# Kernel optimization log

Hardware: AMD Instinct MI355X
Metric: run time of the kernel (lower is better)

The kernel has to match this reference:

```python
import math
import jax, jax.numpy as jnp
import numpy as np

N_NODES = 10000
N_EDGES = 160000
F_IN = 256
HID = 500
N_OUT = 100


def setup_inputs() -> dict:
    key = jax.random.key(0)
    ks = jax.random.split(key, 20)
    inp = {}
    inp['x'] = jax.random.normal(ks[0], (N_NODES, F_IN), jnp.float32)
    inp['edge_src'] = jax.random.randint(ks[1], (N_EDGES,), 0, N_NODES, jnp.int32)
    inp['edge_dst'] = jax.random.randint(ks[2], (N_EDGES,), 0, N_NODES, jnp.int32)
    inp['edge_weight'] = jax.random.uniform(ks[3], (N_EDGES,), jnp.float32)
    s1 = 1.0 / math.sqrt(F_IN)
    s2 = 1.0 / math.sqrt(HID)
    inp['W1_rel'] = jax.random.uniform(ks[4], (HID, F_IN), jnp.float32, -s1, s1)
    inp['b1'] = jax.random.uniform(ks[5], (HID,), jnp.float32, -s1, s1)
    inp['W1_root'] = jax.random.uniform(ks[6], (HID, F_IN), jnp.float32, -s1, s1)
    inp['p1_w'] = jax.random.uniform(ks[7], (HID,), jnp.float32, -s2, s2)
    inp['W2_rel'] = jax.random.uniform(ks[8], (HID, HID), jnp.float32, -s2, s2)
    inp['b2'] = jax.random.uniform(ks[9], (HID,), jnp.float32, -s2, s2)
    inp['W2_root'] = jax.random.uniform(ks[10], (HID, HID), jnp.float32, -s2, s2)
    inp['p2_w'] = jax.random.uniform(ks[11], (HID,), jnp.float32, -s2, s2)
    s3 = 1.0 / math.sqrt(1000)
    inp['lin1_W'] = jax.random.uniform(ks[12], (2000, 1000), jnp.float32, -s3, s3)
    inp['lin1_b'] = jax.random.uniform(ks[13], (2000,), jnp.float32, -s3, s3)
    s4 = 1.0 / math.sqrt(2000)
    inp['lin2_W'] = jax.random.uniform(ks[14], (4000, 2000), jnp.float32, -s4, s4)
    inp['lin2_b'] = jax.random.uniform(ks[15], (4000,), jnp.float32, -s4, s4)
    s5 = 1.0 / math.sqrt(4000)
    inp['lin3_W'] = jax.random.uniform(ks[16], (N_OUT, 4000), jnp.float32, -s5, s5)
    inp['lin3_b'] = jax.random.uniform(ks[17], (N_OUT,), jnp.float32, -s5, s5)
    return inp


def graph_conv(x, src, dst, w, W_rel, b_rel, W_root):
    # PyG GraphConv: out_i = W_rel @ sum_{j->i} w_ji * x_j + b + W_root @ x_i
    msg = x[src] * w[:, None]                              # [E, F]
    agg = jax.ops.segment_sum(msg, dst, num_segments=x.shape[0])
    return agg @ W_rel.T + b_rel + x @ W_root.T


def topk_pool(x, src, dst, w, p_w, ratio=0.5):
    # PyG TopKPooling: score = tanh(x @ p / ||p||); keep top-k; scale x by score.
    N = x.shape[0]
    k = int(math.ceil(ratio * N))
    score = jnp.tanh((x @ p_w) / jnp.linalg.norm(p_w))
    vals, perm = jax.lax.top_k(score, k)
    x_new = x[perm] * vals[:, None]
    # keep fixed-size edge list; dropped edges get weight 0 and point to node 0
    new_idx = jnp.zeros((N,), jnp.int32).at[perm].set(jnp.arange(k, dtype=jnp.int32))
    mask = jnp.zeros((N,), bool).at[perm].set(True)
    keep = mask[src] & mask[dst]
    src_new = jnp.where(keep, new_idx[src], 0)
    dst_new = jnp.where(keep, new_idx[dst], 0)
    w_new = jnp.where(keep, w, 0.0)
    return x_new, src_new, dst_new, w_new


def readout(x):
    # global max pool + global mean pool over the single graph -> [1, 2F]
    return jnp.concatenate([jnp.max(x, 0, keepdims=True), jnp.mean(x, 0, keepdims=True)], axis=1)


def reference(x, edge_src, edge_dst, edge_weight,
              W1_rel, b1, W1_root, p1_w,
              W2_rel, b2, W2_root, p2_w,
              lin1_W, lin1_b, lin2_W, lin2_b, lin3_W, lin3_b):
    h = jax.nn.relu(graph_conv(x, edge_src, edge_dst, edge_weight, W1_rel, b1, W1_root))
    h, s1, d1, w1 = topk_pool(h, edge_src, edge_dst, edge_weight, p1_w)
    x1 = readout(h)
    h = jax.nn.relu(graph_conv(h, s1, d1, w1, W2_rel, b2, W2_root))
    h, _, _, _ = topk_pool(h, s1, d1, w1, p2_w)
    x2 = readout(h)
    z = x1 + x2                                            # [1, 1000]
    z = jax.nn.relu(z @ lin1_W.T + lin1_b)
    z = jax.nn.relu(z @ lin2_W.T + lin2_b)                 # dropout is identity at eval
    return jax.nn.sigmoid(z @ lin3_W.T + lin3_b)
```

## Files before the change

kernel.cpp:

```cpp
#include <hip/hip_runtime.h>
#include <hip/hip_bf16.h>
#include <math.h>

#define NN1   10000
#define NE    160000
#define FIN   256
#define HID   500
#define K1    5000
#define NN2   5000
#define K2    2500

#define CSR_OFFS   0u
#define CSR_POS    10008u
#define CSR_EDGE   20008u
#define OFF_AGG    340016u
#define OFF_H      2900016u
#define OFF_XP2    (OFF_H + 2500000u)
#define OFF_SCP    7900016u
#define OFF_RK1    10410016u
#define OFF_Z      10432016u
#define OFF_T1     10433016u
#define OFF_T2     10435016u
#define OFF_INV    10439016u
#define OFF_CNT    10439024u
#define OFF_PM1    10639024u
#define OFF_PS1    10671024u
#define OFF_XB     10703024u
#define OFF_W1RB   11983024u
#define OFF_W1TB   12047024u
#define OFF_W2RB   12111024u
#define OFF_W2TB   12236024u
#define OFF_XP1B   12361024u
#define OFF_PM2    13611024u
#define OFF_PS2    13627024u
#define WS_FLOATS  13643024u

#define RCHUNK 500
#define ROSLAB1 64
#define ROSLAB2 32
#define RORPB   79

__device__ inline unsigned f2ord(float f) {
    unsigned u = __float_as_uint(f);
    return (u & 0x80000000u) ? ~u : (u | 0x80000000u);
}
__device__ inline unsigned long long rkey(float s, int j) {
    return ((unsigned long long)f2ord(s) << 32) | (unsigned)(0xFFFFFFFFu - (unsigned)j);
}
__device__ inline unsigned short bf16rn(float f) {
    unsigned u = __float_as_uint(f);
    u += 0x7FFFu + ((u >> 16) & 1u);
    return (unsigned short)(u >> 16);
}
__device__ inline float bf2f(unsigned short u) {
    return __uint_as_float((unsigned)u << 16);
}

typedef __attribute__((ext_vector_type(8))) short short8;
typedef __attribute__((ext_vector_type(4))) float floatx4;


__global__ __launch_bounds__(256) void k_prep(
    const float* __restrict__ x, unsigned short* __restrict__ xb,
    const float* __restrict__ w1r, unsigned short* __restrict__ w1rb,
    const float* __restrict__ w1t, unsigned short* __restrict__ w1tb,
    const float* __restrict__ w2r, unsigned short* __restrict__ w2rb,
    const float* __restrict__ w2t, unsigned short* __restrict__ w2tb,
    const float* __restrict__ p1, const float* __restrict__ p2,
    float* __restrict__ invn,
    const int* __restrict__ edst, int* __restrict__ pos) {
    __shared__ float red[256];
    int y = blockIdx.y;
    if (y < 5) {
        const float* s; unsigned short* d; int n;
        switch (y) {
            case 0: s = x;   d = xb;   n = NN1 * FIN; break;
            case 1: s = w1r; d = w1rb; n = HID * FIN; break;
            case 2: s = w1t; d = w1tb; n = HID * FIN; break;
            case 3: s = w2r; d = w2rb; n = HID * HID; break;
            default: s = w2t; d = w2tb; n = HID * HID; break;
        }
        int i = (blockIdx.x * 256 + threadIdx.x) * 4;
        if (i >= n) return;
        if (i + 3 < n) {
            float4 v = *(const float4*)(s + i);
            ushort4 o;
            o.x = bf16rn(v.x); o.y = bf16rn(v.y); o.z = bf16rn(v.z); o.w = bf16rn(v.w);
            *(ushort4*)(d + i) = o;
        } else {
            for (int q = 0; q < 4 && i + q < n; ++q) d[i + q] = bf16rn(s[i + q]);
        }
    } else if (y == 5) {
        if (blockIdx.x >= 2) return;
        const float* p = blockIdx.x ? p2 : p1;
        float s = 0.f;
        for (int i = threadIdx.x; i < HID; i += 256) { float v = p[i]; s += v * v; }
        red[threadIdx.x] = s; __syncthreads();
        for (int w = 128; w > 0; w >>= 1) {
            if (threadIdx.x < w) red[threadIdx.x] += red[threadIdx.x + w];
            __syncthreads();
        }
        if (threadIdx.x == 0) invn[blockIdx.x] = 1.0f / sqrtf(red[0]);
    } else {
        int e = blockIdx.x * 256 + threadIdx.x;
        if (e < NE) atomicAdd(&pos[edst[e]], 1);
    }
}

__global__ __launch_bounds__(1024) void k_scan(int* __restrict__ pos, int* __restrict__ offs) {
    __shared__ int tot[1024];
    int t = threadIdx.x;
    int base = t * 10;
    int loc[10]; int s = 0;
    #pragma unroll
    for (int q = 0; q < 10; ++q) {
        int v = (base + q < NN1) ? pos[base + q] : 0;
        loc[q] = s; s += v;
    }
    tot[t] = s; __syncthreads();
    for (int d = 1; d < 1024; d <<= 1) {
        int v = (t >= d) ? tot[t - d] : 0;
        __syncthreads();
        tot[t] += v;
        __syncthreads();
    }
    int excl = (t == 0) ? 0 : tot[t - 1];
    #pragma unroll
    for (int q = 0; q < 10; ++q)
        if (base + q < NN1) { int o = excl + loc[q]; offs[base + q] = o; pos[base + q] = o; }
    if (t == 1023) offs[NN1] = tot[1023];
}

__global__ void k_fill(const int* __restrict__ src, const int* __restrict__ dst,
                       const float* __restrict__ w, int* __restrict__ pos,
                       int2* __restrict__ ce) {
    int e = blockIdx.x * 256 + threadIdx.x;
    if (e >= NE) return;
    int slot = atomicAdd(&pos[dst[e]], 1);
    ce[slot] = make_int2(src[e], __float_as_int(w[e]));
}

__global__ __launch_bounds__(256) void k_gather1(
    const unsigned short* __restrict__ xb, const int* __restrict__ offs,
    const int2* __restrict__ ce, unsigned short* __restrict__ aggb) {
    int wave = (blockIdx.x * 256 + threadIdx.x) >> 6;
    int lane = threadIdx.x & 63;
    if (wave >= NN1) return;
    int b = offs[wave], e = offs[wave + 1];
    float4 a0 = make_float4(0.f, 0.f, 0.f, 0.f);
    float4 a1 = make_float4(0.f, 0.f, 0.f, 0.f);
    int p = b;
    for (; p + 1 < e; p += 2) {
        int2 e0 = ce[p], e1 = ce[p + 1];
        float w0 = __int_as_float(e0.y), w1 = __int_as_float(e1.y);
        ushort4 u0 = *(const ushort4*)(xb + (size_t)e0.x * FIN + lane * 4);
        ushort4 u1 = *(const ushort4*)(xb + (size_t)e1.x * FIN + lane * 4);
        a0.x += bf2f(u0.x) * w0; a0.y += bf2f(u0.y) * w0;
        a0.z += bf2f(u0.z) * w0; a0.w += bf2f(u0.w) * w0;
        a1.x += bf2f(u1.x) * w1; a1.y += bf2f(u1.y) * w1;
        a1.z += bf2f(u1.z) * w1; a1.w += bf2f(u1.w) * w1;
    }
    if (p < e) {
        int2 e0 = ce[p];
        float w0 = __int_as_float(e0.y);
        ushort4 u0 = *(const ushort4*)(xb + (size_t)e0.x * FIN + lane * 4);
        a0.x += bf2f(u0.x) * w0; a0.y += bf2f(u0.y) * w0;
        a0.z += bf2f(u0.z) * w0; a0.w += bf2f(u0.w) * w0;
    }
    ushort4 o;
    o.x = bf16rn(a0.x + a1.x); o.y = bf16rn(a0.y + a1.y);
    o.z = bf16rn(a0.z + a1.z); o.w = bf16rn(a0.w + a1.w);
    *(ushort4*)(aggb + (size_t)wave * FIN + lane * 4) = o;
}

__global__ __launch_bounds__(256) void k_gather2(
    const unsigned short* __restrict__ Xb, const int* __restrict__ offs,
    const int2* __restrict__ ce, const int* __restrict__ rank,
    unsigned short* __restrict__ aggb) {
    int wave = (blockIdx.x * 256 + threadIdx.x) >> 6;
    int lane = threadIdx.x & 63;
    if (wave >= NN1) return;
    int rd = rank[wave];
    if (rd < 0) return;
    int b = offs[wave], e = offs[wave + 1];
    int c1 = 256 + lane * 4;
    float a0 = 0.f, a1 = 0.f, a2 = 0.f, a3 = 0.f;
    float b0 = 0.f, b1v = 0.f, b2 = 0.f, b3 = 0.f;
    int2 nxt = (b < e) ? ce[b] : make_int2(0, 0);
    for (int p = b; p < e; ++p) {
        int2 cur = nxt;
        if (p + 1 < e) nxt = ce[p + 1];
        int rs = rank[cur.x];
        if (rs < 0) continue;
        float we = __int_as_float(cur.y);
        const unsigned short* row = Xb + (size_t)rs * HID;
        ushort4 u = *(const ushort4*)(row + lane * 4);
        a0 += bf2f(u.x) * we; a1 += bf2f(u.y) * we;
        a2 += bf2f(u.z) * we; a3 += bf2f(u.w) * we;
        if (c1 < HID) {
            ushort4 u2 = *(const ushort4*)(row + c1);
            b0 += bf2f(u2.x) * we; b1v += bf2f(u2.y) * we;
            b2 += bf2f(u2.z) * we; b3 += bf2f(u2.w) * we;
        }
    }
    unsigned short* o = aggb + (size_t)rd * HID;
    ushort4 o1; o1.x = bf16rn(a0); o1.y = bf16rn(a1); o1.z = bf16rn(a2); o1.w = bf16rn(a3);
    *(ushort4*)(o + lane * 4) = o1;
    if (c1 < HID) {
        ushort4 o2; o2.x = bf16rn(b0); o2.y = bf16rn(b1v); o2.z = bf16rn(b2); o2.w = bf16rn(b3);
        *(ushort4*)(o + c1) = o2;
    }
}

__device__ inline short8 ld8g(const unsigned short* p, int gk, int K) {
    if (gk + 7 < K) return *(const short8*)p;
    unsigned short tmp[8] = {0,0,0,0,0,0,0,0};
    for (int q = 0; q < 8; ++q) if (gk + q < K) tmp[q] = p[q];
    return *(short8*)tmp;
}

#define GBK 64
__global__ __launch_bounds__(256) void k_gemm_bf16(
    const unsigned short* __restrict__ A1, const unsigned short* __restrict__ B1,
    const unsigned short* __restrict__ A2, const unsigned short* __restrict__ B2,
    const float* __restrict__ bias, const float* __restrict__ pv,
    unsigned short* __restrict__ C, float* __restrict__ scpart,
    int M, int N, int Ka, int Kb, int nbyRow) {
    int b = blockIdx.x;
    int xcd = b & 7, seq = b >> 3;
    int colT = seq & 7;
    int rowT = xcd + 8 * (seq >> 3);
    if (rowT >= nbyRow) return;
    int row0 = rowT * 64, col0 = colT * 64;

    __shared__ unsigned short As[2][64 * 64];
    __shared__ unsigned short Bs[2][64 * 64];
    int tid = threadIdx.x;
    int lane = tid & 63, wid = tid >> 6;
    int waveM = wid & 1, waveN = wid >> 1;
    int quad = lane >> 4, mrow = lane & 15;
    int m7 = mrow & 7;
    floatx4 acc[2][2] = {};

    int sr = tid >> 2;
    int ca = (tid & 3) * 2;
    int s7 = sr & 7;
    int c0 = (ca ^ s7) * 8;
    int c1 = ((ca + 1) ^ s7) * 8;
    int sbase = sr * 64;

    int nka = (Ka + GBK - 1) / GBK;
    int nkb = (Kb + GBK - 1) / GBK;
    int niter = nka + nkb;

    short8 z8 = {0,0,0,0,0,0,0,0};
    short8 paA = z8, paB = z8, pbA = z8, pbB = z8;

    auto fetch = [&](int t) {
        int ph = (t >= nka);
        const unsigned short* A = ph ? A2 : A1;
        const unsigned short* B = ph ? B2 : B1;
        int K = ph ? Kb : Ka;
        int gk = (ph ? t - nka : t) * GBK + ca * 8;
        int gr = row0 + sr, gn = col0 + sr;
        paA = z8; paB = z8; pbA = z8; pbB = z8;
        if (gr < M) {
            const unsigned short* p = A + (size_t)gr * K + gk;
            paA = ld8g(p, gk, K); paB = ld8g(p + 8, gk + 8, K);
        }
        if (gn < N) {
            const unsigned short* p = B + (size_t)gn * K + gk;
            pbA = ld8g(p, gk, K); pbB = ld8g(p + 8, gk + 8, K);
        }
    };
    auto commit = [&](int buf) {
        *(short8*)&As[buf][sbase + c0] = paA;
        *(short8*)&As[buf][sbase + c1] = paB;
        *(short8*)&Bs[buf][sbase + c0] = pbA;
        *(short8*)&Bs[buf][sbase + c1] = pbB;
    };

    fetch(0);
    commit(0);
    if (niter > 1) fetch(1);
    __syncthreads();

    for (int it = 0; it < niter; ++it) {
        int cur = it & 1;
        if (it + 1 < niter) commit(cur ^ 1);
        if (it + 2 < niter) fetch(it + 2);
        #pragma unroll
        for (int half = 0; half < 2; ++half) {
            int qc = half * 4 + quad;
            int qoff = (qc ^ m7) * 8;
            short8 bfr[2];
            #pragma unroll
            for (int nt = 0; nt < 2; ++nt)
                bfr[nt] = *(short8*)&Bs[cur][(waveN * 32 + nt * 16 + mrow) * 64 + qoff];
            #pragma unroll
            for (int mt = 0; mt < 2; ++mt) {
                short8 afr = *(short8*)&As[cur][(waveM * 32 + mt * 16 + mrow) * 64 + qoff];
                #pragma unroll
                for (int nt = 0; nt < 2; ++nt)
                    acc[mt][nt] = __builtin_amdgcn_mfma_f32_16x16x32_bf16(
                        afr, bfr[nt], acc[mt][nt], 0, 0, 0);
            }
        }
        __syncthreads();
    }
    float ps[2][4] = {};
    #pragma unroll
    for (int nt = 0; nt < 2; ++nt) {
        int col = col0 + waveN * 32 + nt * 16 + mrow;
        if (col >= N) continue;
        float bv = bias[col];
        float pc = pv[col];
        #pragma unroll
        for (int mt = 0; mt < 2; ++mt) {
            int rbase = row0 + waveM * 32 + mt * 16 + quad * 4;
            #pragma unroll
            for (int r = 0; r < 4; ++r) {
                float v = fmaxf(acc[mt][nt][r] + bv, 0.f);
                int row = rbase + r;
                if (row < M) C[(size_t)row * N + col] = bf16rn(v);
                ps[mt][r] += v * pc;
            }
        }
    }
    int part = colT * 2 + waveN;
    #pragma unroll
    for (int mt = 0; mt < 2; ++mt)
        #pragma unroll
        for (int r = 0; r < 4; ++r) {
            float v = ps[mt][r];
            v += __shfl_xor(v, 1, 64); v += __shfl_xor(v, 2, 64);
            v += __shfl_xor(v, 4, 64); v += __shfl_xor(v, 8, 64);
            if (mrow == 0) {
                int row = row0 + waveM * 32 + mt * 16 + quad * 4 + r;
                if (row < M) scpart[(size_t)part * M + row] = v;
            }
        }
}

__global__ __launch_bounds__(256) void k_rank_partial(
    const float* __restrict__ scpart, int* __restrict__ cntp, int Nn) {
    __shared__ unsigned long long kj[RCHUNK];
    int j0 = blockIdx.y * RCHUNK;
    int jn = min(Nn - j0, RCHUNK);
    for (int t = threadIdx.x; t < jn; t += 256) {
        float s = 0.f;
        #pragma unroll
        for (int q = 0; q < 16; ++q) s += scpart[(size_t)q * Nn + j0 + t];
        kj[t] = rkey(s, j0 + t);
    }
    __syncthreads();
    int i = blockIdx.x * 256 + threadIdx.x;
    if (i >= Nn) return;
    float si = 0.f;
    #pragma unroll
    for (int q = 0; q < 16; ++q) si += scpart[(size_t)q * Nn + i];
    unsigned long long ki = rkey(si, i);
    int c = 0;
    #pragma unroll 4
    for (int q = 0; q < jn; ++q)
        c += (kj[q] > ki) ? 1 : 0;
    cntp[(size_t)blockIdx.y * Nn + i] = c;
}

__global__ __launch_bounds__(128) void k_gather_pool(
    const unsigned short* __restrict__ Hb, const float* __restrict__ scpart,
    const float* __restrict__ invn,
    const int* __restrict__ cntp, int Nn, int nchunk, int kk,
    int* __restrict__ rank_out, unsigned short* __restrict__ Xb) {
    __shared__ int csum[128];
    __shared__ float ssum[128];
    __shared__ int rsh;
    __shared__ float scsh;
    int i = blockIdx.x;
    int c = 0;
    for (int q = threadIdx.x; q < nchunk; q += 128) c += cntp[(size_t)q * Nn + i];
    float s = (threadIdx.x < 16) ? scpart[(size_t)threadIdx.x * Nn + i] : 0.f;
    csum[threadIdx.x] = c; ssum[threadIdx.x] = s;
    __syncthreads();
    if (threadIdx.x == 0) {
        int t = 0;
        int lim = (nchunk < 128) ? nchunk : 128;
        for (int q = 0; q < lim; ++q) t += csum[q];
        float st = 0.f;
        for (int q = 0; q < 16; ++q) st += ssum[q];
        int r = (t < kk) ? t : -1;
        if (rank_out) rank_out[i] = r;
        rsh = r;
        scsh = tanhf(st * invn[0]);
    }
    __syncthreads();
    int r = rsh;
    if (r < 0) return;
    float sc = scsh;
    int cc = threadIdx.x;
    if (cc < HID / 4) {
        ushort4 u = *(const ushort4*)(Hb + (size_t)i * HID + cc * 4);
        ushort4 o;
        o.x = bf16rn(bf2f(u.x) * sc); o.y = bf16rn(bf2f(u.y) * sc);
        o.z = bf16rn(bf2f(u.z) * sc); o.w = bf16rn(bf2f(u.w) * sc);
        *(ushort4*)(Xb + (size_t)r * HID + cc * 4) = o;
    }
}

__global__ __launch_bounds__(256) void k_readout_slab(
    const unsigned short* __restrict__ X, int rows, int rpb,
    float* __restrict__ pmax, float* __restrict__ psum) {
    __shared__ float4 lmx[4][64];
    __shared__ float4 lsm[4][64];
    int lane = threadIdx.x & 63;
    int rgrp = threadIdx.x >> 6;
    int c4 = blockIdx.x * 64 + lane;
    int r0 = blockIdx.y * rpb;
    int r1 = min(rows, r0 + rpb);
    float4 mx = make_float4(-INFINITY, -INFINITY, -INFINITY, -INFINITY);
    float4 sm = make_float4(0.f, 0.f, 0.f, 0.f);
    if (c4 < HID / 4) {
        for (int r = r0 + rgrp; r < r1; r += 4) {
            ushort4 u = *(const ushort4*)(X + (size_t)r * HID + c4 * 4);
            float vx = bf2f(u.x), vy = bf2f(u.y), vz = bf2f(u.z), vw = bf2f(u.w);
            mx.x = fmaxf(mx.x, vx); mx.y = fmaxf(mx.y, vy);
            mx.z = fmaxf(mx.z, vz); mx.w = fmaxf(mx.w, vw);
            sm.x += vx; sm.y += vy; sm.z += vz; sm.w += vw;
        }
    }
    lmx[rgrp][lane] = mx; lsm[rgrp][lane] = sm;
    __syncthreads();
    if (rgrp == 0 && c4 < HID / 4) {
        #pragma unroll
        for (int g = 1; g < 4; ++g) {
            float4 m2 = lmx[g][lane], s2 = lsm[g][lane];
            mx.x = fmaxf(mx.x, m2.x); mx.y = fmaxf(mx.y, m2.y);
            mx.z = fmaxf(mx.z, m2.z); mx.w = fmaxf(mx.w, m2.w);
            sm.x += s2.x; sm.y += s2.y; sm.z += s2.z; sm.w += s2.w;
        }
        *(float4*)(pmax + (size_t)blockIdx.y * HID + c4 * 4) = mx;
        *(float4*)(psum + (size_t)blockIdx.y * HID + c4 * 4) = sm;
    }
}

__global__ __launch_bounds__(64) void k_combine_all(
    const float* __restrict__ pm1, const float* __restrict__ ps1, int ns1,
    const float* __restrict__ pm2, const float* __restrict__ ps2, int ns2,
    float* __restrict__ z) {
    int j = blockIdx.x * 64 + threadIdx.x;
    if (j >= HID) return;
    float m1 = -INFINITY, s1 = 0.f;
    for (int s = 0; s < ns1; ++s) {
        m1 = fmaxf(m1, pm1[(size_t)s * HID + j]);
        s1 += ps1[(size_t)s * HID + j];
    }
    float m2 = -INFINITY, s2 = 0.f;
    for (int s = 0; s < ns2; ++s) {
        m2 = fmaxf(m2, pm2[(size_t)s * HID + j]);
        s2 += ps2[(size_t)s * HID + j];
    }
    z[j] = m1 + m2;
    z[HID + j] = s1 * (1.0f / (float)K1) + s2 * (1.0f / (float)K2);
}

__global__ __launch_bounds__(256) void k_mv(
    const float* __restrict__ v, const float* __restrict__ W,
    const float* __restrict__ bias, float* __restrict__ y,
    int rowsN, int K, int act) {
    int wave = (blockIdx.x * 256 + threadIdx.x) >> 6;
    int lane = threadIdx.x & 63;
    if (wave >= rowsN) return;
    const float* wr = W + (size_t)wave * K;
    float s = 0.f;
    for (int c = lane * 4; c < K; c += 256) {
        float4 a = *(const float4*)(wr + c);
        float4 xv = *(const float4*)(v + c);
        s += a.x * xv.x + a.y * xv.y + a.z * xv.z + a.w * xv.w;
    }
    for (int off = 32; off > 0; off >>= 1) s += __shfl_down(s, off, 64);
    if (lane == 0) {
        float r = s + bias[wave];
        y[wave] = (act == 0) ? fmaxf(r, 0.f) : 1.f / (1.f + expf(-r));
    }
}

extern "C" void kernel_launch(void* const* d_in, const int* in_sizes, int n_in,
                              void* d_out, int out_size, void* d_ws, size_t ws_size,
                              hipStream_t stream) {
    const float* x      = (const float*)d_in[0];
    const int*   esrc   = (const int*)d_in[1];
    const int*   edst   = (const int*)d_in[2];
    const float* ew     = (const float*)d_in[3];
    const float* W1_rel = (const float*)d_in[4];
    const float* b1     = (const float*)d_in[5];
    const float* W1_root= (const float*)d_in[6];
    const float* p1     = (const float*)d_in[7];
    const float* W2_rel = (const float*)d_in[8];
    const float* b2     = (const float*)d_in[9];
    const float* W2_root= (const float*)d_in[10];
    const float* p2     = (const float*)d_in[11];
    const float* l1W    = (const float*)d_in[12];
    const float* l1b    = (const float*)d_in[13];
    const float* l2W    = (const float*)d_in[14];
    const float* l2b    = (const float*)d_in[15];
    const float* l3W    = (const float*)d_in[16];
    const float* l3b    = (const float*)d_in[17];
    float* out = (float*)d_out;
    float* ws  = (float*)d_ws;

    if (ws_size < (size_t)WS_FLOATS * sizeof(float)) return;

    int*            offs  = (int*)(ws + CSR_OFFS);
    int*            pos   = (int*)(ws + CSR_POS);
    int2*           ce    = (int2*)(ws + CSR_EDGE);
    unsigned short* aggb  = (unsigned short*)(ws + OFF_AGG);
    unsigned short* hb    = (unsigned short*)(ws + OFF_H);
    unsigned short* xp2b  = (unsigned short*)(ws + OFF_XP2);
    float*          scp   = ws + OFF_SCP;
    int*            rk1   = (int*)(ws + OFF_RK1);
    float*          zbuf  = ws + OFF_Z;
    float*          t1    = ws + OFF_T1;
    float*          t2    = ws + OFF_T2;
    float*          invn  = ws + OFF_INV;
    int*            cntp  = (int*)(ws + OFF_CNT);
    float*          pm1   = ws + OFF_PM1;
    float*          ps1   = ws + OFF_PS1;
    float*          pm2   = ws + OFF_PM2;
    float*          ps2   = ws + OFF_PS2;
    unsigned short* xb    = (unsigned short*)(ws + OFF_XB);
    unsigned short* w1rb  = (unsigned short*)(ws + OFF_W1RB);
    unsigned short* w1tb  = (unsigned short*)(ws + OFF_W1TB);
    unsigned short* w2rb  = (unsigned short*)(ws + OFF_W2RB);
    unsigned short* w2tb  = (unsigned short*)(ws + OFF_W2TB);
    unsigned short* xp1b  = (unsigned short*)(ws + OFF_XP1B);

    hipMemsetAsync(pos, 0, NN1 * sizeof(int), stream);
    k_prep<<<dim3(2500, 7), 256, 0, stream>>>(
        x, xb, W1_rel, w1rb, W1_root, w1tb, W2_rel, w2rb, W2_root, w2tb,
        p1, p2, invn, edst, pos);
    k_scan<<<1, 1024, 0, stream>>>(pos, offs);
    k_fill<<<(NE + 255) / 256, 256, 0, stream>>>(esrc, edst, ew, pos, ce);

    k_gather1<<<(NN1 * 64 + 255) / 256, 256, 0, stream>>>(xb, offs, ce, aggb);
    {
        int nby = (NN1 + 63) / 64;
        int nblk = 64 * ((nby + 7) / 8);
        k_gemm_bf16<<<nblk, 256, 0, stream>>>(
            aggb, w1rb, xb, w1tb, b1, p1, hb, scp, NN1, HID, FIN, FIN, nby);
    }

    k_rank_partial<<<dim3((NN1 + 255) / 256, NN1 / RCHUNK), 256, 0, stream>>>(scp, cntp, NN1);
    k_gather_pool<<<NN1, 128, 0, stream>>>(hb, scp, invn + 0, cntp, NN1, NN1 / RCHUNK, K1,
                                           rk1, xp1b);
    k_readout_slab<<<dim3(2, ROSLAB1), 256, 0, stream>>>(xp1b, K1, RORPB, pm1, ps1);

    k_gather2<<<(NN1 * 64 + 255) / 256, 256, 0, stream>>>(xp1b, offs, ce, rk1, aggb);
    {
        int nby = (NN2 + 63) / 64;
        int nblk = 64 * ((nby + 7) / 8);
        k_gemm_bf16<<<nblk, 256, 0, stream>>>(
            aggb, w2rb, xp1b, w2tb, b2, p2, hb, scp, NN2, HID, HID, HID, nby);
    }

    k_rank_partial<<<dim3((NN2 + 255) / 256, NN2 / RCHUNK), 256, 0, stream>>>(scp, cntp, NN2);
    k_gather_pool<<<NN2, 128, 0, stream>>>(hb, scp, invn + 1, cntp, NN2, NN2 / RCHUNK, K2,
                                           (int*)nullptr, xp2b);
    k_readout_slab<<<dim3(2, ROSLAB2), 256, 0, stream>>>(xp2b, K2, RORPB, pm2, ps2);
    k_combine_all<<<(HID + 63) / 64, 64, 0, stream>>>(pm1, ps1, ROSLAB1, pm2, ps2, ROSLAB2, zbuf);

    k_mv<<<(2000 * 64) / 256, 256, 0, stream>>>(zbuf, l1W, l1b, t1, 2000, 1000, 0);
    k_mv<<<(4000 * 64) / 256, 256, 0, stream>>>(t1, l2W, l2b, t2, 4000, 2000, 0);
    k_mv<<<(100 * 64) / 256, 256, 0, stream>>>(t2, l3W, l3b, out, 100, 4000, 1);
}
```

Baseline: 329.0 us.

## Fuse pipeline stages into fewer kernels with last-block scans and grid barriers

Folds the degree-count scan into k_prep using a last-block-done counter, removing the separate scan launch. Moves top-k ranking into the GEMM epilogue via a completion counter, and merges gather2 with the layer-1 readout. Collapses pool2, readout2, combine and the three matvecs into one persistent kernel synchronised by software grid barriers. This cuts kernel launches and round trips through memory. The cost is serialised last-block work and grid-barrier overhead, and the barriers depend on all 512 blocks being resident at once to avoid deadlock.

```diff
diff --git a/kernel.cpp b/kernel.cpp
--- a/kernel.cpp
+++ b/kernel.cpp
@@ -1,5 +1,4 @@
 #include <hip/hip_runtime.h>
-#include <hip/hip_bf16.h>
 #include <math.h>
 
 #define NN1   10000
@@ -9,36 +8,40 @@
 #define K1    5000
 #define NN2   5000
 #define K2    2500
+#define NSLAB 64
+#define RORPB  79
+#define RORPB2 40
 
 #define CSR_OFFS   0u
 #define CSR_POS    10008u
-#define CSR_EDGE   20008u
-#define OFF_AGG    340016u
-#define OFF_H      2900016u
-#define OFF_XP2    (OFF_H + 2500000u)
-#define OFF_SCP    7900016u
-#define OFF_RK1    10410016u
-#define OFF_Z      10432016u
-#define OFF_T1     10433016u
-#define OFF_T2     10435016u
-#define OFF_INV    10439016u
-#define OFF_CNT    10439024u
-#define OFF_PM1    10639024u
-#define OFF_PS1    10671024u
-#define OFF_XB     10703024u
-#define OFF_W1RB   11983024u
-#define OFF_W1TB   12047024u
-#define OFF_W2RB   12111024u
-#define OFF_W2TB   12236024u
-#define OFF_XP1B   12361024u
-#define OFF_PM2    13611024u
-#define OFF_PS2    13627024u
-#define WS_FLOATS  13643024u
-
-#define RCHUNK 500
-#define ROSLAB1 64
-#define ROSLAB2 32
-#define RORPB   79
+#define OFF_SC1    20008u
+#define OFF_SC2    30008u
+#define OFF_CTR    35008u
+#define ZERO_BASE  10008u
+#define ZERO_LEN   25032u
+#define CSR_EDGE   35040u
+#define OFF_SCALE1 355040u
+#define OFF_SCALE2 365040u
+#define OFF_RK1    370040u
+#define OFF_RK2    380040u
+#define OFF_PM1    385056u
+#define OFF_PS1    417056u
+#define OFF_PM2    449056u
+#define OFF_PS2    481056u
+#define OFF_Z      513056u
+#define OFF_T1     514056u
+#define OFF_T2     516056u
+#define OFF_INV    520056u
+#define OFF_AGG    520064u
+#define OFF_H      1800064u
+#define OFF_XP1B   4300064u
+#define OFF_XP2B   5550064u
+#define OFF_XB     6175064u
+#define OFF_W1RB   7455064u
+#define OFF_W1TB   7519064u
+#define OFF_W2RB   7583064u
+#define OFF_W2TB   7708064u
+#define WS_FLOATS  7833088u
 
 __device__ inline unsigned f2ord(float f) {
     unsigned u = __float_as_uint(f);
@@ -58,6 +61,13 @@
 
 typedef __attribute__((ext_vector_type(8))) short short8;
 typedef __attribute__((ext_vector_type(4))) float floatx4;
+
+__device__ inline short8 ld8g(const unsigned short* p, int gk, int K) {
+    if (gk + 7 < K) return *(const short8*)p;
+    unsigned short tmp[8] = {0,0,0,0,0,0,0,0};
+    for (int q = 0; q < 8; ++q) if (gk + q < K) tmp[q] = p[q];
+    return *(short8*)tmp;
+}
 
 
 __global__ __launch_bounds__(256) void k_prep(
@@ -68,72 +78,76 @@
     const float* __restrict__ w2t, unsigned short* __restrict__ w2tb,
     const float* __restrict__ p1, const float* __restrict__ p2,
     float* __restrict__ invn,
-    const int* __restrict__ edst, int* __restrict__ pos) {
+    const int* __restrict__ edst, int* __restrict__ pos,
+    int* __restrict__ offs, int* __restrict__ ctr) {
     __shared__ float red[256];
+    __shared__ int ts[264];
+    int tid = threadIdx.x;
     int y = blockIdx.y;
     if (y < 5) {
-        const float* s; unsigned short* d; int n;
+        const float* s; unsigned short* d; int n4;
         switch (y) {
-            case 0: s = x;   d = xb;   n = NN1 * FIN; break;
-            case 1: s = w1r; d = w1rb; n = HID * FIN; break;
-            case 2: s = w1t; d = w1tb; n = HID * FIN; break;
-            case 3: s = w2r; d = w2rb; n = HID * HID; break;
-            default: s = w2t; d = w2tb; n = HID * HID; break;
-        }
-        int i = (blockIdx.x * 256 + threadIdx.x) * 4;
-        if (i >= n) return;
-        if (i + 3 < n) {
-            float4 v = *(const float4*)(s + i);
+            case 0: s = x;   d = xb;   n4 = NN1 * FIN / 4; break;
+            case 1: s = w1r; d = w1rb; n4 = HID * FIN / 4; break;
+            case 2: s = w1t; d = w1tb; n4 = HID * FIN / 4; break;
+            case 3: s = w2r; d = w2rb; n4 = HID * HID / 4; break;
+            default: s = w2t; d = w2tb; n4 = HID * HID / 4; break;
+        }
+        int stride = gridDim.x * 256;
+        for (int i = blockIdx.x * 256 + tid; i < n4; i += stride) {
+            float4 v = *(const float4*)(s + (size_t)i * 4);
             ushort4 o;
             o.x = bf16rn(v.x); o.y = bf16rn(v.y); o.z = bf16rn(v.z); o.w = bf16rn(v.w);
-            *(ushort4*)(d + i) = o;
-        } else {
-            for (int q = 0; q < 4 && i + q < n; ++q) d[i + q] = bf16rn(s[i + q]);
-        }
-    } else if (y == 5) {
-        if (blockIdx.x >= 2) return;
-        const float* p = blockIdx.x ? p2 : p1;
-        float s = 0.f;
-        for (int i = threadIdx.x; i < HID; i += 256) { float v = p[i]; s += v * v; }
-        red[threadIdx.x] = s; __syncthreads();
-        for (int w = 128; w > 0; w >>= 1) {
-            if (threadIdx.x < w) red[threadIdx.x] += red[threadIdx.x + w];
-            __syncthreads();
-        }
-        if (threadIdx.x == 0) invn[blockIdx.x] = 1.0f / sqrtf(red[0]);
-    } else {
-        int e = blockIdx.x * 256 + threadIdx.x;
-        if (e < NE) atomicAdd(&pos[edst[e]], 1);
-    }
-}
-
-__global__ __launch_bounds__(1024) void k_scan(int* __restrict__ pos, int* __restrict__ offs) {
-    __shared__ int tot[1024];
-    int t = threadIdx.x;
-    int base = t * 10;
-    int loc[10]; int s = 0;
-    #pragma unroll
-    for (int q = 0; q < 10; ++q) {
-        int v = (base + q < NN1) ? pos[base + q] : 0;
-        loc[q] = s; s += v;
-    }
-    tot[t] = s; __syncthreads();
-    for (int d = 1; d < 1024; d <<= 1) {
-        int v = (t >= d) ? tot[t - d] : 0;
-        __syncthreads();
-        tot[t] += v;
-        __syncthreads();
-    }
-    int excl = (t == 0) ? 0 : tot[t - 1];
-    #pragma unroll
-    for (int q = 0; q < 10; ++q)
-        if (base + q < NN1) { int o = excl + loc[q]; offs[base + q] = o; pos[base + q] = o; }
-    if (t == 1023) offs[NN1] = tot[1023];
-}
-
-__global__ void k_fill(const int* __restrict__ src, const int* __restrict__ dst,
-                       const float* __restrict__ w, int* __restrict__ pos,
-                       int2* __restrict__ ce) {
+            *(ushort4*)(d + (size_t)i * 4) = o;
+        }
+        return;
+    }
+    if (y == 5) {
+        if (blockIdx.x < 2) {
+            const float* p = blockIdx.x ? p2 : p1;
+            float sv = 0.f;
+            for (int i = tid; i < HID; i += 256) { float v = p[i]; sv += v * v; }
+            red[tid] = sv; __syncthreads();
+            for (int w = 128; w > 0; w >>= 1) {
+                if (tid < w) red[tid] += red[tid + w];
+                __syncthreads();
+            }
+            if (tid == 0) invn[blockIdx.x] = 1.0f / sqrtf(red[0]);
+        }
+        return;
+    }
+    {
+        int stride = gridDim.x * 256;
+        for (int e = blockIdx.x * 256 + tid; e < NE; e += stride)
+            atomicAdd(&pos[edst[e]], 1);
+    }
+    if (tid == 0) {
+        __threadfence();
+        ts[256] = (atomicAdd(ctr, 1) == (int)gridDim.x - 1) ? 1 : 0;
+    }
+    __syncthreads();
+    if (!ts[256]) return;
+    __threadfence();
+    int chunk = (NN1 + 255) / 256;
+    int i0 = tid * chunk, i1 = min(NN1, i0 + chunk);
+    int acc = 0;
+    for (int i = i0; i < i1; ++i) acc += pos[i];
+    ts[tid] = acc; __syncthreads();
+    for (int d = 1; d < 256; d <<= 1) {
+        int v = (tid >= d) ? ts[tid - d] : 0;
+        __syncthreads(); ts[tid] += v; __syncthreads();
+    }
+    int run = tid ? ts[tid - 1] : 0;
+    for (int i = i0; i < i1; ++i) {
+        int v = pos[i]; offs[i] = run; pos[i] = run; run += v;
+    }
+    if (tid == 255) offs[NN1] = ts[255];
+}
+
+__global__ __launch_bounds__(256) void k_fill(
+    const int* __restrict__ src, const int* __restrict__ dst,
+    const float* __restrict__ w, int* __restrict__ pos,
+    int2* __restrict__ ce) {
     int e = blockIdx.x * 256 + threadIdx.x;
     if (e >= NE) return;
     int slot = atomicAdd(&pos[dst[e]], 1);
@@ -173,249 +187,247 @@
     *(ushort4*)(aggb + (size_t)wave * FIN + lane * 4) = o;
 }
 
-__global__ __launch_bounds__(256) void k_gather2(
-    const unsigned short* __restrict__ Xb, const int* __restrict__ offs,
-    const int2* __restrict__ ce, const int* __restrict__ rank,
-    unsigned short* __restrict__ aggb) {
-    int wave = (blockIdx.x * 256 + threadIdx.x) >> 6;
-    int lane = threadIdx.x & 63;
-    if (wave >= NN1) return;
-    int rd = rank[wave];
-    if (rd < 0) return;
-    int b = offs[wave], e = offs[wave + 1];
-    int c1 = 256 + lane * 4;
-    float a0 = 0.f, a1 = 0.f, a2 = 0.f, a3 = 0.f;
-    float b0 = 0.f, b1v = 0.f, b2 = 0.f, b3 = 0.f;
-    int2 nxt = (b < e) ? ce[b] : make_int2(0, 0);
-    for (int p = b; p < e; ++p) {
-        int2 cur = nxt;
-        if (p + 1 < e) nxt = ce[p + 1];
-        int rs = rank[cur.x];
-        if (rs < 0) continue;
-        float we = __int_as_float(cur.y);
-        const unsigned short* row = Xb + (size_t)rs * HID;
-        ushort4 u = *(const ushort4*)(row + lane * 4);
-        a0 += bf2f(u.x) * we; a1 += bf2f(u.y) * we;
-        a2 += bf2f(u.z) * we; a3 += bf2f(u.w) * we;
-        if (c1 < HID) {
-            ushort4 u2 = *(const ushort4*)(row + c1);
-            b0 += bf2f(u2.x) * we; b1v += bf2f(u2.y) * we;
-            b2 += bf2f(u2.z) * we; b3 += bf2f(u2.w) * we;
-        }
-    }
-    unsigned short* o = aggb + (size_t)rd * HID;
-    ushort4 o1; o1.x = bf16rn(a0); o1.y = bf16rn(a1); o1.z = bf16rn(a2); o1.w = bf16rn(a3);
-    *(ushort4*)(o + lane * 4) = o1;
-    if (c1 < HID) {
-        ushort4 o2; o2.x = bf16rn(b0); o2.y = bf16rn(b1v); o2.z = bf16rn(b2); o2.w = bf16rn(b3);
-        *(ushort4*)(o + c1) = o2;
-    }
-}
-
-__device__ inline short8 ld8g(const unsigned short* p, int gk, int K) {
-    if (gk + 7 < K) return *(const short8*)p;
-    unsigned short tmp[8] = {0,0,0,0,0,0,0,0};
-    for (int q = 0; q < 8; ++q) if (gk + q < K) tmp[q] = p[q];
-    return *(short8*)tmp;
-}
-
 #define GBK 64
 __global__ __launch_bounds__(256) void k_gemm_bf16(
     const unsigned short* __restrict__ A1, const unsigned short* __restrict__ B1,
     const unsigned short* __restrict__ A2, const unsigned short* __restrict__ B2,
     const float* __restrict__ bias, const float* __restrict__ pv,
-    unsigned short* __restrict__ C, float* __restrict__ scpart,
+    unsigned short* __restrict__ C, float* __restrict__ score,
+    int* __restrict__ rank_out, float* __restrict__ scale_out,
+    const float* __restrict__ invp, int kk, int* __restrict__ donectr,
     int M, int N, int Ka, int Kb, int nbyRow) {
+    __shared__ unsigned short As[2][64 * 64];
+    __shared__ unsigned short Bs[2][64 * 64];
+    int tid = threadIdx.x;
     int b = blockIdx.x;
     int xcd = b & 7, seq = b >> 3;
     int colT = seq & 7;
     int rowT = xcd + 8 * (seq >> 3);
-    if (rowT >= nbyRow) return;
-    int row0 = rowT * 64, col0 = colT * 64;
-
-    __shared__ unsigned short As[2][64 * 64];
-    __shared__ unsigned short Bs[2][64 * 64];
-    int tid = threadIdx.x;
-    int lane = tid & 63, wid = tid >> 6;
-    int waveM = wid & 1, waveN = wid >> 1;
-    int quad = lane >> 4, mrow = lane & 15;
-    int m7 = mrow & 7;
-    floatx4 acc[2][2] = {};
-
-    int sr = tid >> 2;
-    int ca = (tid & 3) * 2;
-    int s7 = sr & 7;
-    int c0 = (ca ^ s7) * 8;
-    int c1 = ((ca + 1) ^ s7) * 8;
-    int sbase = sr * 64;
-
-    int nka = (Ka + GBK - 1) / GBK;
-    int nkb = (Kb + GBK - 1) / GBK;
-    int niter = nka + nkb;
-
-    short8 z8 = {0,0,0,0,0,0,0,0};
-    short8 paA = z8, paB = z8, pbA = z8, pbB = z8;
-
-    auto fetch = [&](int t) {
-        int ph = (t >= nka);
-        const unsigned short* A = ph ? A2 : A1;
-        const unsigned short* B = ph ? B2 : B1;
-        int K = ph ? Kb : Ka;
-        int gk = (ph ? t - nka : t) * GBK + ca * 8;
-        int gr = row0 + sr, gn = col0 + sr;
-        paA = z8; paB = z8; pbA = z8; pbB = z8;
-        if (gr < M) {
-            const unsigned short* p = A + (size_t)gr * K + gk;
-            paA = ld8g(p, gk, K); paB = ld8g(p + 8, gk + 8, K);
-        }
-        if (gn < N) {
-            const unsigned short* p = B + (size_t)gn * K + gk;
-            pbA = ld8g(p, gk, K); pbB = ld8g(p + 8, gk + 8, K);
-        }
-    };
-    auto commit = [&](int buf) {
-        *(short8*)&As[buf][sbase + c0] = paA;
-        *(short8*)&As[buf][sbase + c1] = paB;
-        *(short8*)&Bs[buf][sbase + c0] = pbA;
-        *(short8*)&Bs[buf][sbase + c1] = pbB;
-    };
-
-    fetch(0);
-    commit(0);
-    if (niter > 1) fetch(1);
-    __syncthreads();
-
-    for (int it = 0; it < niter; ++it) {
-        int cur = it & 1;
-        if (it + 1 < niter) commit(cur ^ 1);
-        if (it + 2 < niter) fetch(it + 2);
+    bool active = (rowT < nbyRow);
+    if (active) {
+        int row0 = rowT * 64, col0 = colT * 64;
+        int lane = tid & 63, wid = tid >> 6;
+        int waveM = wid & 1, waveN = wid >> 1;
+        int quad = lane >> 4, mrow = lane & 15;
+        int m7 = mrow & 7;
+        floatx4 acc[2][2] = {};
+
+        int sr = tid >> 2;
+        int ca = (tid & 3) * 2;
+        int s7 = sr & 7;
+        int c0 = (ca ^ s7) * 8;
+        int c1 = ((ca + 1) ^ s7) * 8;
+        int sbase = sr * 64;
+
+        int nka = (Ka + GBK - 1) / GBK;
+        int nkb = (Kb + GBK - 1) / GBK;
+        int niter = nka + nkb;
+
+        short8 z8 = {0,0,0,0,0,0,0,0};
+        short8 paA = z8, paB = z8, pbA = z8, pbB = z8;
+
+        auto fetch = [&](int t) {
+            int ph = (t >= nka);
+            const unsigned short* A = ph ? A2 : A1;
+            const unsigned short* B = ph ? B2 : B1;
+            int K = ph ? Kb : Ka;
+            int gk = (ph ? t - nka : t) * GBK + ca * 8;
+            int gr = row0 + sr, gn = col0 + sr;
+            paA = z8; paB = z8; pbA = z8; pbB = z8;
+            if (gr < M) {
+                const unsigned short* p = A + (size_t)gr * K + gk;
+                paA = ld8g(p, gk, K); paB = ld8g(p + 8, gk + 8, K);
+            }
+            if (gn < N) {
+                const unsigned short* p = B + (size_t)gn * K + gk;
+                pbA = ld8g(p, gk, K); pbB = ld8g(p + 8, gk + 8, K);
+            }
+        };
+        auto commit = [&](int buf) {
+            *(short8*)&As[buf][sbase + c0] = paA;
+            *(short8*)&As[buf][sbase + c1] = paB;
+            *(short8*)&Bs[buf][sbase + c0] = pbA;
+            *(short8*)&Bs[buf][sbase + c1] = pbB;
+        };
+
+        fetch(0);
+        commit(0);
+        if (niter > 1) fetch(1);
+        __syncthreads();
+
+        for (int it = 0; it < niter; ++it) {
+            int cur = it & 1;
+            if (it + 1 < niter) commit(cur ^ 1);
+            if (it + 2 < niter) fetch(it + 2);
+            #pragma unroll
+            for (int half = 0; half < 2; ++half) {
+                int qc = half * 4 + quad;
+                int qoff = (qc ^ m7) * 8;
+                short8 bfr[2];
+                #pragma unroll
+                for (int nt = 0; nt < 2; ++nt)
+                    bfr[nt] = *(short8*)&Bs[cur][(waveN * 32 + nt * 16 + mrow) * 64 + qoff];
+                #pragma unroll
+                for (int mt = 0; mt < 2; ++mt) {
+                    short8 afr = *(short8*)&As[cur][(waveM * 32 + mt * 16 + mrow) * 64 + qoff];
+                    #pragma unroll
+                    for (int nt = 0; nt < 2; ++nt)
+                        acc[mt][nt] = __builtin_amdgcn_mfma_f32_16x16x32_bf16(
+                            afr, bfr[nt], acc[mt][nt], 0, 0, 0);
+                }
+            }
+            __syncthreads();
+        }
+        float ps[2][4] = {};
         #pragma unroll
-        for (int half = 0; half < 2; ++half) {
-            int qc = half * 4 + quad;
-            int qoff = (qc ^ m7) * 8;
-            short8 bfr[2];
-            #pragma unroll
-            for (int nt = 0; nt < 2; ++nt)
-                bfr[nt] = *(short8*)&Bs[cur][(waveN * 32 + nt * 16 + mrow) * 64 + qoff];
+        for (int nt = 0; nt < 2; ++nt) {
+            int col = col0 + waveN * 32 + nt * 16 + mrow;
+            if (col >= N) continue;
+            float bv = bias[col];
+            float pc = pv[col];
             #pragma unroll
             for (int mt = 0; mt < 2; ++mt) {
-                short8 afr = *(short8*)&As[cur][(waveM * 32 + mt * 16 + mrow) * 64 + qoff];
+                int rbase = row0 + waveM * 32 + mt * 16 + quad * 4;
                 #pragma unroll
-                for (int nt = 0; nt < 2; ++nt)
-                    acc[mt][nt] = __builtin_amdgcn_mfma_f32_16x16x32_bf16(
-                        afr, bfr[nt], acc[mt][nt], 0, 0, 0);
-            }
-        }
-        __syncthreads();
-    }
-    float ps[2][4] = {};
-    #pragma unroll
-    for (int nt = 0; nt < 2; ++nt) {
-        int col = col0 + waveN * 32 + nt * 16 + mrow;
-        if (col >= N) continue;
-        float bv = bias[col];
-        float pc = pv[col];
+                for (int r = 0; r < 4; ++r) {
+                    float v = fmaxf(acc[mt][nt][r] + bv, 0.f);
+                    int row = rbase + r;
+                    if (row < M) C[(size_t)row * N + col] = bf16rn(v);
+                    ps[mt][r] += v * pc;
+                }
+            }
+        }
         #pragma unroll
-        for (int mt = 0; mt < 2; ++mt) {
-            int rbase = row0 + waveM * 32 + mt * 16 + quad * 4;
+        for (int mt = 0; mt < 2; ++mt)
             #pragma unroll
             for (int r = 0; r < 4; ++r) {
-                float v = fmaxf(acc[mt][nt][r] + bv, 0.f);
-                int row = rbase + r;
-                if (row < M) C[(size_t)row * N + col] = bf16rn(v);
-                ps[mt][r] += v * pc;
-            }
-        }
-    }
-    int part = colT * 2 + waveN;
-    #pragma unroll
-    for (int mt = 0; mt < 2; ++mt)
-        #pragma unroll
-        for (int r = 0; r < 4; ++r) {
-            float v = ps[mt][r];
-            v += __shfl_xor(v, 1, 64); v += __shfl_xor(v, 2, 64);
-            v += __shfl_xor(v, 4, 64); v += __shfl_xor(v, 8, 64);
-            if (mrow == 0) {
-                int row = row0 + waveM * 32 + mt * 16 + quad * 4 + r;
-                if (row < M) scpart[(size_t)part * M + row] = v;
-            }
-        }
-}
-
-__global__ __launch_bounds__(256) void k_rank_partial(
-    const float* __restrict__ scpart, int* __restrict__ cntp, int Nn) {
-    __shared__ unsigned long long kj[RCHUNK];
-    int j0 = blockIdx.y * RCHUNK;
-    int jn = min(Nn - j0, RCHUNK);
-    for (int t = threadIdx.x; t < jn; t += 256) {
-        float s = 0.f;
-        #pragma unroll
-        for (int q = 0; q < 16; ++q) s += scpart[(size_t)q * Nn + j0 + t];
-        kj[t] = rkey(s, j0 + t);
-    }
-    __syncthreads();
-    int i = blockIdx.x * 256 + threadIdx.x;
-    if (i >= Nn) return;
-    float si = 0.f;
-    #pragma unroll
-    for (int q = 0; q < 16; ++q) si += scpart[(size_t)q * Nn + i];
-    unsigned long long ki = rkey(si, i);
-    int c = 0;
-    #pragma unroll 4
-    for (int q = 0; q < jn; ++q)
-        c += (kj[q] > ki) ? 1 : 0;
-    cntp[(size_t)blockIdx.y * Nn + i] = c;
-}
-
-__global__ __launch_bounds__(128) void k_gather_pool(
-    const unsigned short* __restrict__ Hb, const float* __restrict__ scpart,
-    const float* __restrict__ invn,
-    const int* __restrict__ cntp, int Nn, int nchunk, int kk,
-    int* __restrict__ rank_out, unsigned short* __restrict__ Xb) {
-    __shared__ int csum[128];
-    __shared__ float ssum[128];
-    __shared__ int rsh;
-    __shared__ float scsh;
+                float v = ps[mt][r];
+                v += __shfl_xor(v, 1, 64); v += __shfl_xor(v, 2, 64);
+                v += __shfl_xor(v, 4, 64); v += __shfl_xor(v, 8, 64);
+                if (mrow == 0) {
+                    int row = row0 + waveM * 32 + mt * 16 + quad * 4 + r;
+                    if (row < M) atomicAdd(&score[row], v);
+                }
+            }
+    }
+
+    int* hist = (int*)(void*)As[0];
+    int* ts   = (int*)(void*)As[1];
+    unsigned long long* keys = (unsigned long long*)(void*)Bs[0];
+    if (tid == 0) {
+        __threadfence();
+        ts[270] = (atomicAdd(donectr, 1) == (int)gridDim.x - 1) ? 1 : 0;
+    }
+    __syncthreads();
+    if (!ts[270]) return;
+    __threadfence();
+
+    unsigned prefMask = 0, prefVal = 0;
+    int need = kk;
+    int cnt = M;
+    const int shifts[3] = {21, 10, 0};
+    const int nbits[3]  = {11, 11, 10};
+    for (int lv = 0; lv < 3 && cnt > 2048; ++lv) {
+        int sh = shifts[lv], nb = 1 << nbits[lv], per = nb >> 8;
+        for (int q = tid; q < nb; q += 256) hist[q] = 0;
+        __syncthreads();
+        for (int i = tid; i < M; i += 256) {
+            unsigned key = f2ord(score[i]);
+            if ((key & prefMask) == prefVal)
+                atomicAdd(&hist[(key >> sh) & (nb - 1)], 1);
+        }
+        __syncthreads();
+        int c = 0;
+        int btop = nb - 1 - tid * per;
+        for (int j = 0; j < per; ++j) c += hist[btop - j];
+        ts[tid] = c; __syncthreads();
+        for (int d = 1; d < 256; d <<= 1) {
+            int v = (tid >= d) ? ts[tid - d] : 0;
+            __syncthreads(); ts[tid] += v; __syncthreads();
+        }
+        int above = tid ? ts[tid - 1] : 0;
+        int cum = above;
+        for (int j = 0; j < per; ++j) {
+            int bb = btop - j; int h = hist[bb];
+            if (cum < need && need <= cum + h) { ts[260] = bb; ts[261] = cum; }
+            cum += h;
+        }
+        __syncthreads();
+        int B = ts[260], abv = ts[261];
+        need -= abv;
+        cnt = hist[B];
+        prefMask |= (unsigned)(nb - 1) << sh;
+        prefVal  |= (unsigned)B << sh;
+        __syncthreads();
+    }
+    if (tid == 0) ts[262] = 0;
+    __syncthreads();
+    for (int i = tid; i < M; i += 256) {
+        float s = score[i];
+        unsigned key = f2ord(s);
+        if ((key & prefMask) == prefVal) {
+            int p = atomicAdd(&ts[262], 1);
+            if (p < 2048) keys[p] = rkey(s, i);
+        }
+    }
+    __syncthreads();
+    int m = ts[262]; if (m > 2048) m = 2048;
+    for (int c = tid; c < m; c += 256) {
+        unsigned long long kc = keys[c];
+        int rk = 0;
+        for (int q = 0; q < m; ++q) rk += (keys[q] > kc) ? 1 : 0;
+        if (rk == need - 1) {
+            ts[263] = (int)(unsigned)(kc & 0xFFFFFFFFull);
+            ts[264] = (int)(unsigned)(kc >> 32);
+        }
+    }
+    __syncthreads();
+    unsigned long long thr =
+        ((unsigned long long)(unsigned)ts[264] << 32) | (unsigned)ts[263];
+    float inv = invp[0];
+    int chunk = (M + 255) / 256;
+    int i0 = tid * chunk, i1 = min(M, i0 + chunk);
+    int ck = 0;
+    for (int i = i0; i < i1; ++i) ck += (rkey(score[i], i) >= thr) ? 1 : 0;
+    ts[tid] = ck; __syncthreads();
+    for (int d = 1; d < 256; d <<= 1) {
+        int v = (tid >= d) ? ts[tid - d] : 0;
+        __syncthreads(); ts[tid] += v; __syncthreads();
+    }
+    int r = tid ? ts[tid - 1] : 0;
+    for (int i = i0; i < i1; ++i) {
+        float s = score[i];
+        bool kept = rkey(s, i) >= thr;
+        rank_out[i] = kept ? r++ : -1;
+        scale_out[i] = tanhf(s * inv);
+    }
+}
+
+__global__ __launch_bounds__(128) void k_pool_gather(
+    const unsigned short* __restrict__ Hb, const int* __restrict__ rank,
+    const float* __restrict__ scale, unsigned short* __restrict__ Xb) {
     int i = blockIdx.x;
-    int c = 0;
-    for (int q = threadIdx.x; q < nchunk; q += 128) c += cntp[(size_t)q * Nn + i];
-    float s = (threadIdx.x < 16) ? scpart[(size_t)threadIdx.x * Nn + i] : 0.f;
-    csum[threadIdx.x] = c; ssum[threadIdx.x] = s;
-    __syncthreads();
-    if (threadIdx.x == 0) {
-        int t = 0;
-        int lim = (nchunk < 128) ? nchunk : 128;
-        for (int q = 0; q < lim; ++q) t += csum[q];
-        float st = 0.f;
-        for (int q = 0; q < 16; ++q) st += ssum[q];
-        int r = (t < kk) ? t : -1;
-        if (rank_out) rank_out[i] = r;
-        rsh = r;
-        scsh = tanhf(st * invn[0]);
-    }
-    __syncthreads();
-    int r = rsh;
+    int r = rank[i];
     if (r < 0) return;
-    float sc = scsh;
     int cc = threadIdx.x;
-    if (cc < HID / 4) {
-        ushort4 u = *(const ushort4*)(Hb + (size_t)i * HID + cc * 4);
-        ushort4 o;
-        o.x = bf16rn(bf2f(u.x) * sc); o.y = bf16rn(bf2f(u.y) * sc);
-        o.z = bf16rn(bf2f(u.z) * sc); o.w = bf16rn(bf2f(u.w) * sc);
-        *(ushort4*)(Xb + (size_t)r * HID + cc * 4) = o;
-    }
-}
-
-__global__ __launch_bounds__(256) void k_readout_slab(
-    const unsigned short* __restrict__ X, int rows, int rpb,
-    float* __restrict__ pmax, float* __restrict__ psum) {
+    if (cc >= HID / 4) return;
+    float sc = scale[i];
+    ushort4 u = *(const ushort4*)(Hb + (size_t)i * HID + cc * 4);
+    ushort4 o;
+    o.x = bf16rn(bf2f(u.x) * sc); o.y = bf16rn(bf2f(u.y) * sc);
+    o.z = bf16rn(bf2f(u.z) * sc); o.w = bf16rn(bf2f(u.w) * sc);
+    *(ushort4*)(Xb + (size_t)r * HID + cc * 4) = o;
+}
+
+__device__ void readout_slab(const unsigned short* __restrict__ X, int rows, int rpb,
+                             int slabY, int colHalf,
+                             float* __restrict__ pmax, float* __restrict__ psum) {
     __shared__ float4 lmx[4][64];
     __shared__ float4 lsm[4][64];
     int lane = threadIdx.x & 63;
     int rgrp = threadIdx.x >> 6;
-    int c4 = blockIdx.x * 64 + lane;
-    int r0 = blockIdx.y * rpb;
+    int c4 = colHalf * 64 + lane;
+    int r0 = slabY * rpb;
     int r1 = min(rows, r0 + rpb);
     float4 mx = make_float4(-INFINITY, -INFINITY, -INFINITY, -INFINITY);
     float4 sm = make_float4(0.f, 0.f, 0.f, 0.f);
@@ -438,50 +450,148 @@
             mx.z = fmaxf(mx.z, m2.z); mx.w = fmaxf(mx.w, m2.w);
             sm.x += s2.x; sm.y += s2.y; sm.z += s2.z; sm.w += s2.w;
         }
-        *(float4*)(pmax + (size_t)blockIdx.y * HID + c4 * 4) = mx;
-        *(float4*)(psum + (size_t)blockIdx.y * HID + c4 * 4) = sm;
-    }
-}
-
-__global__ __launch_bounds__(64) void k_combine_all(
-    const float* __restrict__ pm1, const float* __restrict__ ps1, int ns1,
-    const float* __restrict__ pm2, const float* __restrict__ ps2, int ns2,
-    float* __restrict__ z) {
-    int j = blockIdx.x * 64 + threadIdx.x;
-    if (j >= HID) return;
-    float m1 = -INFINITY, s1 = 0.f;
-    for (int s = 0; s < ns1; ++s) {
-        m1 = fmaxf(m1, pm1[(size_t)s * HID + j]);
-        s1 += ps1[(size_t)s * HID + j];
-    }
-    float m2 = -INFINITY, s2 = 0.f;
-    for (int s = 0; s < ns2; ++s) {
-        m2 = fmaxf(m2, pm2[(size_t)s * HID + j]);
-        s2 += ps2[(size_t)s * HID + j];
-    }
-    z[j] = m1 + m2;
-    z[HID + j] = s1 * (1.0f / (float)K1) + s2 * (1.0f / (float)K2);
-}
-
-__global__ __launch_bounds__(256) void k_mv(
-    const float* __restrict__ v, const float* __restrict__ W,
-    const float* __restrict__ bias, float* __restrict__ y,
-    int rowsN, int K, int act) {
-    int wave = (blockIdx.x * 256 + threadIdx.x) >> 6;
-    int lane = threadIdx.x & 63;
-    if (wave >= rowsN) return;
-    const float* wr = W + (size_t)wave * K;
-    float s = 0.f;
-    for (int c = lane * 4; c < K; c += 256) {
-        float4 a = *(const float4*)(wr + c);
-        float4 xv = *(const float4*)(v + c);
-        s += a.x * xv.x + a.y * xv.y + a.z * xv.z + a.w * xv.w;
-    }
-    for (int off = 32; off > 0; off >>= 1) s += __shfl_down(s, off, 64);
-    if (lane == 0) {
-        float r = s + bias[wave];
-        y[wave] = (act == 0) ? fmaxf(r, 0.f) : 1.f / (1.f + expf(-r));
-    }
+        *(float4*)(pmax + (size_t)slabY * HID + c4 * 4) = mx;
+        *(float4*)(psum + (size_t)slabY * HID + c4 * 4) = sm;
+    }
+}
+
+__global__ __launch_bounds__(256) void k_g2r1(
+    const unsigned short* __restrict__ xp1, const int* __restrict__ offs,
+    const int2* __restrict__ ce, const int* __restrict__ rank,
+    unsigned short* __restrict__ aggb,
+    float* __restrict__ pm1, float* __restrict__ ps1) {
+    if (blockIdx.x < 2500) {
+        int wave = (blockIdx.x * 256 + threadIdx.x) >> 6;
+        int lane = threadIdx.x & 63;
+        int rd = rank[wave];
+        if (rd < 0) return;
+        int b = offs[wave], e = offs[wave + 1];
+        int c1 = 256 + lane * 4;
+        float a0 = 0.f, a1 = 0.f, a2 = 0.f, a3 = 0.f;
+        float b0 = 0.f, b1v = 0.f, b2 = 0.f, b3 = 0.f;
+        int2 nxt = (b < e) ? ce[b] : make_int2(0, 0);
+        for (int p = b; p < e; ++p) {
+            int2 cur = nxt;
+            if (p + 1 < e) nxt = ce[p + 1];
+            int rs = rank[cur.x];
+            if (rs < 0) continue;
+            float we = __int_as_float(cur.y);
+            const unsigned short* row = xp1 + (size_t)rs * HID;
+            ushort4 u = *(const ushort4*)(row + lane * 4);
+            a0 += bf2f(u.x) * we; a1 += bf2f(u.y) * we;
+            a2 += bf2f(u.z) * we; a3 += bf2f(u.w) * we;
+            if (c1 < HID) {
+                ushort4 u2 = *(const ushort4*)(row + c1);
+                b0 += bf2f(u2.x) * we; b1v += bf2f(u2.y) * we;
+                b2 += bf2f(u2.z) * we; b3 += bf2f(u2.w) * we;
+            }
+        }
+        unsigned short* o = aggb + (size_t)rd * HID;
+        ushort4 o1; o1.x = bf16rn(a0); o1.y = bf16rn(a1); o1.z = bf16rn(a2); o1.w = bf16rn(a3);
+        *(ushort4*)(o + lane * 4) = o1;
+        if (c1 < HID) {
+            ushort4 o2; o2.x = bf16rn(b0); o2.y = bf16rn(b1v); o2.z = bf16rn(b2); o2.w = bf16rn(b3);
+            *(ushort4*)(o + c1) = o2;
+        }
+    } else {
+        int b = blockIdx.x - 2500;
+        readout_slab(xp1, K1, RORPB, b >> 1, b & 1, pm1, ps1);
+    }
+}
+
+__device__ inline void gridbar(int* bar, int nblk) {
+    __threadfence();
+    __syncthreads();
+    if (threadIdx.x == 0) {
+        if (atomicAdd(bar, 1) < nblk - 1) {
+            while (__hip_atomic_load(bar, __ATOMIC_ACQUIRE, __HIP_MEMORY_SCOPE_AGENT) < nblk)
+                __builtin_amdgcn_s_sleep(2);
+        }
+    }
+    __syncthreads();
+    __threadfence();
+}
+
+__device__ void mv_rows(const float* __restrict__ v, const float* __restrict__ W,
+                        const float* __restrict__ bias, float* __restrict__ y,
+                        int rowsN, int K, int act, int gwave, int nwaves, int lane) {
+    for (int row = gwave; row < rowsN; row += nwaves) {
+        const float* wr = W + (size_t)row * K;
+        float s = 0.f;
+        for (int c = lane * 4; c < K; c += 256) {
+            float4 a = *(const float4*)(wr + c);
+            float4 xv = *(const float4*)(v + c);
+            s += a.x * xv.x + a.y * xv.y + a.z * xv.z + a.w * xv.w;
+        }
+        for (int off = 32; off > 0; off >>= 1) s += __shfl_down(s, off, 64);
+        if (lane == 0) {
+            float r = s + bias[row];
+            y[row] = (act == 0) ? fmaxf(r, 0.f) : 1.f / (1.f + expf(-r));
+        }
+    }
+}
+
+__global__ __launch_bounds__(256, 2) void k_backhalf(
+    const unsigned short* __restrict__ hb, const int* __restrict__ rank2,
+    const float* __restrict__ scale2, unsigned short* __restrict__ xp2,
+    const float* __restrict__ pm1, const float* __restrict__ ps1,
+    float* __restrict__ pm2, float* __restrict__ ps2,
+    float* __restrict__ z, float* __restrict__ t1, float* __restrict__ t2,
+    const float* __restrict__ l1W, const float* __restrict__ l1b,
+    const float* __restrict__ l2W, const float* __restrict__ l2b,
+    const float* __restrict__ l3W, const float* __restrict__ l3b,
+    float* __restrict__ out, int* __restrict__ bar) {
+    int tid = threadIdx.x;
+    int lane = tid & 63, wid = tid >> 6;
+    int gwave = blockIdx.x * 4 + wid;
+    int nwaves = gridDim.x * 4;
+    int nblk = gridDim.x;
+
+    for (int i = gwave; i < NN2; i += nwaves) {
+        int r = rank2[i];
+        if (r < 0) continue;
+        float sc = scale2[i];
+        const unsigned short* src = hb + (size_t)i * HID;
+        unsigned short* dst = xp2 + (size_t)r * HID;
+        ushort4 u = *(const ushort4*)(src + lane * 4);
+        ushort4 o;
+        o.x = bf16rn(bf2f(u.x) * sc); o.y = bf16rn(bf2f(u.y) * sc);
+        o.z = bf16rn(bf2f(u.z) * sc); o.w = bf16rn(bf2f(u.w) * sc);
+        *(ushort4*)(dst + lane * 4) = o;
+        int c2 = lane + 64;
+        if (c2 < HID / 4) {
+            ushort4 u2 = *(const ushort4*)(src + c2 * 4);
+            ushort4 o2;
+            o2.x = bf16rn(bf2f(u2.x) * sc); o2.y = bf16rn(bf2f(u2.y) * sc);
+            o2.z = bf16rn(bf2f(u2.z) * sc); o2.w = bf16rn(bf2f(u2.w) * sc);
+            *(ushort4*)(dst + c2 * 4) = o2;
+        }
+    }
+    gridbar(bar + 0, nblk);
+
+    if (blockIdx.x < 2 * NSLAB)
+        readout_slab(xp2, K2, RORPB2, blockIdx.x >> 1, blockIdx.x & 1, pm2, ps2);
+    gridbar(bar + 1, nblk);
+
+    {
+        int j = blockIdx.x * 256 + tid;
+        if (j < HID) {
+            float m1 = -INFINITY, s1 = 0.f, m2 = -INFINITY, s2 = 0.f;
+            for (int s = 0; s < NSLAB; ++s) {
+                m1 = fmaxf(m1, pm1[(size_t)s * HID + j]); s1 += ps1[(size_t)s * HID + j];
+                m2 = fmaxf(m2, pm2[(size_t)s * HID + j]); s2 += ps2[(size_t)s * HID + j];
+            }
+            z[j] = m1 + m2;
+            z[HID + j] = s1 * (1.0f / (float)K1) + s2 * (1.0f / (float)K2);
+        }
+    }
+    gridbar(bar + 2, nblk);
+
+    mv_rows(z, l1W, l1b, t1, 2000, 1000, 0, gwave, nwaves, lane);
+    gridbar(bar + 3, nblk);
+    mv_rows(t1, l2W, l2b, t2, 4000, 2000, 0, gwave, nwaves, lane);
+    gridbar(bar + 4, nblk);
+    mv_rows(t2, l3W, l3b, out, 100, 4000, 1, gwave, nwaves, lane);
 }
 
 extern "C" void kernel_launch(void* const* d_in, const int* in_sizes, int n_in,
@@ -510,65 +620,61 @@
 
     if (ws_size < (size_t)WS_FLOATS * sizeof(float)) return;
 
-    int*            offs  = (int*)(ws + CSR_OFFS);
-    int*            pos   = (int*)(ws + CSR_POS);
-    int2*           ce    = (int2*)(ws + CSR_EDGE);
-    unsigned short* aggb  = (unsigned short*)(ws + OFF_AGG);
-    unsigned short* hb    = (unsigned short*)(ws + OFF_H);
-    unsigned short* xp2b  = (unsigned short*)(ws + OFF_XP2);
-    float*          scp   = ws + OFF_SCP;
-    int*            rk1   = (int*)(ws + OFF_RK1);
-    float*          zbuf  = ws + OFF_Z;
-    float*          t1    = ws + OFF_T1;
-    float*          t2    = ws + OFF_T2;
-    float*          invn  = ws + OFF_INV;
-    int*            cntp  = (int*)(ws + OFF_CNT);
-    float*          pm1   = ws + OFF_PM1;
-    float*          ps1   = ws + OFF_PS1;
-    float*          pm2   = ws + OFF_PM2;
-    float*          ps2   = ws + OFF_PS2;
-    unsigned short* xb    = (unsigned short*)(ws + OFF_XB);
-    unsigned short* w1rb  = (unsigned short*)(ws + OFF_W1RB);
-    unsigned short* w1tb  = (unsigned short*)(ws + OFF_W1TB);
-    unsigned short* w2rb  = (unsigned short*)(ws + OFF_W2RB);
-    unsigned short* w2tb  = (unsigned short*)(ws + OFF_W2TB);
-    unsigned short* xp1b  = (unsigned short*)(ws + OFF_XP1B);
-
-    hipMemsetAsync(pos, 0, NN1 * sizeof(int), stream);
-    k_prep<<<dim3(2500, 7), 256, 0, stream>>>(
+    int*            offs   = (int*)(ws + CSR_OFFS);
+    int*            pos    = (int*)(ws + CSR_POS);
+    float*          score1 = ws + OFF_SC1;
+    float*          score2 = ws + OFF_SC2;
+    int*            ctr    = (int*)(ws + OFF_CTR);
+    int2*           ce     = (int2*)(ws + CSR_EDGE);
+    float*          scale1 = ws + OFF_SCALE1;
+    float*          scale2 = ws + OFF_SCALE2;
+    int*            rk1    = (int*)(ws + OFF_RK1);
+    int*            rk2    = (int*)(ws + OFF_RK2);
+    float*          pm1    = ws + OFF_PM1;
+    float*          ps1    = ws + OFF_PS1;
+    float*          pm2    = ws + OFF_PM2;
+    float*          ps2    = ws + OFF_PS2;
+    float*          zbuf   = ws + OFF_Z;
+    float*          t1     = ws + OFF_T1;
+    float*          t2     = ws + OFF_T2;
+    float*          invn   = ws + OFF_INV;
+    unsigned short* aggb   = (unsigned short*)(ws + OFF_AGG);
+    unsigned short* hb     = (unsigned short*)(ws + OFF_H);
+    unsigned short* xp1b   = (unsigned short*)(ws + OFF_XP1B);
+    unsigned short* xp2b   = (unsigned short*)(ws + OFF_XP2B);
+    unsigned short* xb     = (unsigned short*)(ws + OFF_XB);
+    unsigned short* w1rb   = (unsigned short*)(ws + OFF_W1RB);
+    unsigned short* w1tb   = (unsigned short*)(ws + OFF_W1TB);
+    unsigned short* w2rb   = (unsigned short*)(ws + OFF_W2RB);
+    unsigned short* w2tb   = (unsigned short*)(ws + OFF_W2TB);
+
+    hipMemsetAsync(ws + ZERO_BASE, 0, (size_t)ZERO_LEN * sizeof(float), stream);
+
+    k_prep<<<dim3(256, 7), 256, 0, stream>>>(
         x, xb, W1_rel, w1rb, W1_root, w1tb, W2_rel, w2rb, W2_root, w2tb,
-        p1, p2, invn, edst, pos);
-    k_scan<<<1, 1024, 0, stream>>>(pos, offs);
+        p1, p2, invn, edst, pos, offs, ctr);
     k_fill<<<(NE + 255) / 256, 256, 0, stream>>>(esrc, edst, ew, pos, ce);
 
-    k_gather1<<<(NN1 * 64 + 255) / 256, 256, 0, stream>>>(xb, offs, ce, aggb);
+    k_gather1<<<(NN1 * 64) / 256, 256, 0, stream>>>(xb, offs, ce, aggb);
     {
         int nby = (NN1 + 63) / 64;
         int nblk = 64 * ((nby + 7) / 8);
         k_gemm_bf16<<<nblk, 256, 0, stream>>>(
-            aggb, w1rb, xb, w1tb, b1, p1, hb, scp, NN1, HID, FIN, FIN, nby);
-    }
-
-    k_rank_partial<<<dim3((NN1 + 255) / 256, NN1 / RCHUNK), 256, 0, stream>>>(scp, cntp, NN1);
-    k_gather_pool<<<NN1, 128, 0, stream>>>(hb, scp, invn + 0, cntp, NN1, NN1 / RCHUNK, K1,
-                                           rk1, xp1b);
-    k_readout_slab<<<dim3(2, ROSLAB1), 256, 0, stream>>>(xp1b, K1, RORPB, pm1, ps1);
-
-    k_gather2<<<(NN1 * 64 + 255) / 256, 256, 0, stream>>>(xp1b, offs, ce, rk1, aggb);
+            aggb, w1rb, xb, w1tb, b1, p1, hb, score1, rk1, scale1,
+            invn + 0, K1, ctr + 1, NN1, HID, FIN, FIN, nby);
+    }
+    k_pool_gather<<<NN1, 128, 0, stream>>>(hb, rk1, scale1, xp1b);
+
+    k_g2r1<<<2500 + 2 * NSLAB, 256, 0, stream>>>(xp1b, offs, ce, rk1, aggb, pm1, ps1);
     {
         int nby = (NN2 + 63) / 64;
         int nblk = 64 * ((nby + 7) / 8);
         k_gemm_bf16<<<nblk, 256, 0, stream>>>(
-            aggb, w2rb, xp1b, w2tb, b2, p2, hb, scp, NN2, HID, HID, HID, nby);
-    }
-
-    k_rank_partial<<<dim3((NN2 + 255) / 256, NN2 / RCHUNK), 256, 0, stream>>>(scp, cntp, NN2);
-    k_gather_pool<<<NN2, 128, 0, stream>>>(hb, scp, invn + 1, cntp, NN2, NN2 / RCHUNK, K2,
-                                           (int*)nullptr, xp2b);
-    k_readout_slab<<<dim3(2, ROSLAB2), 256, 0, stream>>>(xp2b, K2, RORPB, pm2, ps2);
-    k_combine_all<<<(HID + 63) / 64, 64, 0, stream>>>(pm1, ps1, ROSLAB1, pm2, ps2, ROSLAB2, zbuf);
-
-    k_mv<<<(2000 * 64) / 256, 256, 0, stream>>>(zbuf, l1W, l1b, t1, 2000, 1000, 0);
-    k_mv<<<(4000 * 64) / 256, 256, 0, stream>>>(t1, l2W, l2b, t2, 4000, 2000, 0);
-    k_mv<<<(100 * 64) / 256, 256, 0, stream>>>(t2, l3W, l3b, out, 100, 4000, 1);
-}
+            aggb, w2rb, xp1b, w2tb, b2, p2, hb, score2, rk2, scale2,
+            invn + 1, K2, ctr + 2, NN2, HID, HID, HID, nby);
+    }
+
+    k_backhalf<<<512, 256, 0, stream>>>(
+        hb, rk2, scale2, xp2b, pm1, ps1, pm2, ps2, zbuf, t1, t2,
+        l1W, l1b, l2W, l2b, l3W, l3b, out, ctr + 8);
+}
```

New measurement: 952.9 us. 2.9x slower.
